# Kernel optimization log

Measured on AMD Instinct MI355X. Metric: run time of the kernel, lower is better.

Reference implementation:

```python
import jax, jax.numpy as jnp
import numpy as np

B, L, D, H = 2, 2048, 1024, 16
HD = D // H


def _xavier(key, out_f, in_f):
    std = (2.0 / (in_f + out_f)) ** 0.5
    return jax.random.normal(key, (out_f, in_f), dtype=jnp.float32) * std


def setup_inputs() -> dict:
    key = jax.random.key(0)
    k = jax.random.split(key, 8)
    Q = jax.random.normal(k[0], (B, L, D), dtype=jnp.float32)
    K = jax.random.normal(k[1], (B, L, D), dtype=jnp.float32)
    V = jax.random.normal(k[2], (B, L, D), dtype=jnp.float32)
    mask = jnp.tril(jnp.ones((L, L), dtype=jnp.int32))[None, None]  # causal [1,1,L,L]
    wq = _xavier(k[3], D, D)
    wk = _xavier(k[4], D, D)
    wv = _xavier(k[5], D, D)
    wo = _xavier(k[6], D, D)
    bo = jnp.zeros((D,), dtype=jnp.float32)
    return {"Q": Q, "K": K, "V": V, "mask": mask,
            "wq": wq, "wk": wk, "wv": wv, "wo": wo, "bo": bo}


def reference(Q, K, V, mask, wq, wk, wv, wo, bo):
    N, Lq, Dm = Q.shape
    # projections: X @ W^T (Linear stores [out, in])
    q = (Q @ wq.T).reshape(N, Lq, H, HD).transpose(0, 2, 1, 3)  # [N,H,L,hd]
    kk = (K @ wk.T).reshape(N, Lq, H, HD).transpose(0, 2, 1, 3)
    v = (V @ wv.T).reshape(N, Lq, H, HD).transpose(0, 2, 1, 3)
    score = jnp.einsum('bhqd,bhkd->bhqk', q, kk) / jnp.sqrt(jnp.float32(HD))
    score = jnp.where(mask == 0, -jnp.inf, score)
    weights = jax.nn.softmax(score, axis=-1)
    attn = jnp.einsum('bhqk,bhkd->bhqd', weights, v)
    out = attn.transpose(0, 2, 1, 3).reshape(N, Lq, Dm)
    return out @ wo.T + bo
```

## Files before the change

kernel.cpp:

```cpp
#include <hip/hip_runtime.h>
#include <hip/hip_bf16.h>


#define B_ 2
#define L_ 2048
#define D_ 1024
#define H_ 16
#define HD_ 64
#define NA_ ((size_t)B_ * L_ * D_)
#define NW_ ((size_t)D_ * D_)

typedef __attribute__((ext_vector_type(8))) short bf16x8;
typedef __attribute__((ext_vector_type(4))) float f32x4;
typedef __hip_bfloat16 bf16;

__device__ __forceinline__ void async_load16(const void* g, void* l) {
  __builtin_amdgcn_global_load_lds((const __attribute__((address_space(1))) void*)g,
                                   (__attribute__((address_space(3))) void*)l,
                                   16, 0, 0);
}

__global__ __launch_bounds__(256) void xcvt_kernel(const float* __restrict__ q,
                                                   const float* __restrict__ k,
                                                   const float* __restrict__ v,
                                                   const float* __restrict__ w0,
                                                   const float* __restrict__ w1,
                                                   const float* __restrict__ w2,
                                                   const float* __restrict__ w3,
                                                   bf16* __restrict__ dst) {
  const int y = blockIdx.y;
  const float* src = (y == 0) ? q : (y == 1) ? k : (y == 2) ? v
                   : (y == 3) ? w0 : (y == 4) ? w1 : (y == 5) ? w2 : w3;
  const size_t n = (y < 3) ? NA_ : NW_;
  const size_t off = (y < 3) ? (size_t)y * NA_ : 3 * NA_ + (size_t)(y - 3) * NW_;
  size_t i = ((size_t)blockIdx.x * 256 + threadIdx.x) * 4;
  if (i >= n) return;
  float4 vv = *(const float4*)(src + i);
  union { bf16 h[4]; uint2 u; } pk;
  pk.h[0] = __float2bfloat16(vv.x);
  pk.h[1] = __float2bfloat16(vv.y);
  pk.h[2] = __float2bfloat16(vv.z);
  pk.h[3] = __float2bfloat16(vv.w);
  *(uint2*)(dst + off + i) = pk.u;
}

__global__ __launch_bounds__(256) void gemm_qkv(const bf16* __restrict__ Qb,
                                                const bf16* __restrict__ Kb,
                                                const bf16* __restrict__ Vb,
                                                const bf16* __restrict__ Wb,
                                                bf16* __restrict__ qp,
                                                bf16* __restrict__ kp,
                                                bf16* __restrict__ vtp) {
  __shared__ __align__(16) bf16 As[128 * 32];
  __shared__ __align__(16) bf16 Bs[128 * 32];
  const int tid = threadIdx.x;
  const int wv = tid >> 6, lane = tid & 63;
  const int quad = lane >> 4, l16 = lane & 15;
  const int wm = wv & 1, wn = wv >> 1;
  const int m0 = blockIdx.x * 128, n0 = blockIdx.y * 128;
  const int z = blockIdx.z;
  const bf16* X = (z == 0) ? Qb : (z == 1) ? Kb : Vb;
  const bf16* W = Wb + (size_t)z * NW_;

  f32x4 acc[4][4];
#pragma unroll
  for (int i = 0; i < 4; i++)
#pragma unroll
    for (int j = 0; j < 4; j++) acc[i][j] = (f32x4){0.f, 0.f, 0.f, 0.f};

  for (int k0 = 0; k0 < D_; k0 += 32) {
#pragma unroll
    for (int it = 0; it < 2; it++) {
      int c = (wv * 2 + it) * 64 + lane;
      int row = c >> 2, cc = c & 3;
      async_load16(X + (size_t)(m0 + row) * D_ + k0 + cc * 8, (char*)As + c * 16);
      async_load16(W + (size_t)(n0 + row) * D_ + k0 + cc * 8, (char*)Bs + c * 16);
    }
    __syncthreads();
    bf16x8 af[4], bfr[4];
#pragma unroll
    for (int mi = 0; mi < 4; mi++)
      af[mi] = *(const bf16x8*)&As[(wm * 64 + mi * 16 + l16) * 32 + quad * 8];
#pragma unroll
    for (int ni = 0; ni < 4; ni++)
      bfr[ni] = *(const bf16x8*)&Bs[(wn * 64 + ni * 16 + l16) * 32 + quad * 8];
#pragma unroll
    for (int mi = 0; mi < 4; mi++)
#pragma unroll
      for (int ni = 0; ni < 4; ni++)
        acc[mi][ni] = __builtin_amdgcn_mfma_f32_16x16x32_bf16(af[mi], bfr[ni],
                                                              acc[mi][ni], 0, 0, 0);
    __syncthreads();
  }

  const float sc = (z == 0) ? 0.125f : 1.0f;
#pragma unroll
  for (int mi = 0; mi < 4; mi++) {
#pragma unroll
    for (int ni = 0; ni < 4; ni++) {
      int n = n0 + wn * 64 + ni * 16 + l16;
#pragma unroll
      for (int r = 0; r < 4; r++) {
        int m = m0 + wm * 64 + mi * 16 + quad * 4 + r;
        bf16 v = __float2bfloat16(acc[mi][ni][r] * sc);
        if (z == 2) {
          int b = m >> 11, l = m & (L_ - 1);
          int h = n >> 6, hd = n & 63;
          vtp[((size_t)((b * H_ + h) * HD_ + hd)) * L_ + l] = v;
        } else {
          ((z == 0) ? qp : kp)[(size_t)m * D_ + n] = v;
        }
      }
    }
  }
}

__global__ __launch_bounds__(256) void attn_kernel(const bf16* __restrict__ qp,
                                                   const bf16* __restrict__ kp,
                                                   const bf16* __restrict__ vt,
                                                   bf16* __restrict__ attn) {
  __shared__ __align__(16) bf16 Kt[2][64 * 64];
  __shared__ __align__(16) bf16 Vt[2][64 * 64];
  __shared__ __align__(16) bf16 Pl[4][16 * 72];
  __shared__ __align__(16) bf16 Ph[4][16 * 72];
  const int tid = threadIdx.x;
  const int wv = tid >> 6, lane = tid & 63;
  const int quad = lane >> 4, l16 = lane & 15;
  const int pair = blockIdx.x, h = blockIdx.y, b = blockIdx.z;
  const int qlo = pair, qhi = (L_ / 64 - 1) - pair;

  const int rL = qlo * 64 + wv * 16 + l16;
  const int rH = qhi * 64 + wv * 16 + l16;
  bf16x8 qaL[2], qaH[2];
#pragma unroll
  for (int kk = 0; kk < 2; kk++) {
    qaL[kk] = *(const bf16x8*)&qp[((size_t)(b * L_ + rL)) * D_ + h * HD_ +
                                  kk * 32 + quad * 8];
    qaH[kk] = *(const bf16x8*)&qp[((size_t)(b * L_ + rH)) * D_ + h * HD_ +
                                  kk * 32 + quad * 8];
  }

  f32x4 OL[4], OH[4];
#pragma unroll
  for (int t = 0; t < 4; t++) {
    OL[t] = (f32x4){0.f, 0.f, 0.f, 0.f};
    OH[t] = (f32x4){0.f, 0.f, 0.f, 0.f};
  }
  float lL[4] = {0.f, 0.f, 0.f, 0.f}, lH[4] = {0.f, 0.f, 0.f, 0.f};

  const int csw = quad ^ (l16 & 7);

  auto stage = [&](int j, int buf) {
    const int j0 = j * 64;
#pragma unroll
    for (int it = 0; it < 2; it++) {
      int slot = (wv * 2 + it) * 64 + lane;
      int row = slot >> 3, c = (slot & 7) ^ (row & 7);
      async_load16(kp + ((size_t)(b * L_ + j0 + row)) * D_ + h * HD_ + c * 8,
                   (char*)Kt[buf] + slot * 16);
      async_load16(vt + ((size_t)((b * H_ + h) * HD_ + row)) * L_ + j0 + c * 8,
                   (char*)Vt[buf] + slot * 16);
    }
  };

  stage(0, 0);
  for (int j = 0; j <= qhi; j++) {
    const int buf = j & 1;
    const int j0 = j * 64;
    const bool doLo = (j <= qlo);
    __syncthreads();
    if (j < qhi) stage(j + 1, buf ^ 1);

    f32x4 sL[4], sH[4];
#pragma unroll
    for (int ss = 0; ss < 4; ss++) {
      int krow = ss * 16 + l16;
      bf16x8 kb0 = *(const bf16x8*)&Kt[buf][krow * 64 + csw * 8];
      bf16x8 kb1 = *(const bf16x8*)&Kt[buf][krow * 64 + (csw ^ 4) * 8];
      f32x4 s = (f32x4){0.f, 0.f, 0.f, 0.f};
      s = __builtin_amdgcn_mfma_f32_16x16x32_bf16(qaH[0], kb0, s, 0, 0, 0);
      s = __builtin_amdgcn_mfma_f32_16x16x32_bf16(qaH[1], kb1, s, 0, 0, 0);
      sH[ss] = s;
      if (doLo) {
        f32x4 t = (f32x4){0.f, 0.f, 0.f, 0.f};
        t = __builtin_amdgcn_mfma_f32_16x16x32_bf16(qaL[0], kb0, t, 0, 0, 0);
        t = __builtin_amdgcn_mfma_f32_16x16x32_bf16(qaL[1], kb1, t, 0, 0, 0);
        sL[ss] = t;
      }
    }

    if (j == qhi) {
#pragma unroll
      for (int ss = 0; ss < 4; ss++) {
        int key = j0 + ss * 16 + l16;
#pragma unroll
        for (int r = 0; r < 4; r++) {
          int rq = qhi * 64 + wv * 16 + quad * 4 + r;
          if (key > rq) sH[ss][r] = -1e30f;
        }
      }
    }
    if (doLo && j == qlo) {
#pragma unroll
      for (int ss = 0; ss < 4; ss++) {
        int key = j0 + ss * 16 + l16;
#pragma unroll
        for (int r = 0; r < 4; r++) {
          int rq = qlo * 64 + wv * 16 + quad * 4 + r;
          if (key > rq) sL[ss][r] = -1e30f;
        }
      }
    }
#pragma unroll
    for (int ss = 0; ss < 4; ss++) {
#pragma unroll
      for (int r = 0; r < 4; r++) {
        float p = __expf(sH[ss][r]);
        lH[r] += p;
        Ph[wv][(quad * 4 + r) * 72 + ss * 16 + l16] = __float2bfloat16(p);
      }
    }
    if (doLo) {
#pragma unroll
      for (int ss = 0; ss < 4; ss++) {
#pragma unroll
        for (int r = 0; r < 4; r++) {
          float p = __expf(sL[ss][r]);
          lL[r] += p;
          Pl[wv][(quad * 4 + r) * 72 + ss * 16 + l16] = __float2bfloat16(p);
        }
      }
    }

    asm volatile("s_waitcnt lgkmcnt(0)" ::: "memory");

#pragma unroll
    for (int kk = 0; kk < 2; kk++) {
      bf16x8 pah = *(const bf16x8*)&Ph[wv][l16 * 72 + kk * 32 + quad * 8];
      bf16x8 pal;
      if (doLo) pal = *(const bf16x8*)&Pl[wv][l16 * 72 + kk * 32 + quad * 8];
#pragma unroll
      for (int t = 0; t < 4; t++) {
        bf16x8 vb = *(const bf16x8*)&Vt[buf][(t * 16 + l16) * 64 + (csw ^ (kk * 4)) * 8];
        OH[t] = __builtin_amdgcn_mfma_f32_16x16x32_bf16(pah, vb, OH[t], 0, 0, 0);
        if (doLo) OL[t] = __builtin_amdgcn_mfma_f32_16x16x32_bf16(pal, vb, OL[t], 0, 0, 0);
      }
    }
  }

#pragma unroll
  for (int r = 0; r < 4; r++) {
#pragma unroll
    for (int off = 1; off < 16; off <<= 1) {
      lL[r] += __shfl_xor(lL[r], off, 64);
      lH[r] += __shfl_xor(lH[r], off, 64);
    }
  }
#pragma unroll
  for (int t = 0; t < 4; t++) {
#pragma unroll
    for (int r = 0; r < 4; r++) {
      int rowL = qlo * 64 + wv * 16 + quad * 4 + r;
      int rowH = qhi * 64 + wv * 16 + quad * 4 + r;
      attn[((size_t)(b * L_ + rowL)) * D_ + h * HD_ + t * 16 + l16] =
          __float2bfloat16(OL[t][r] / lL[r]);
      attn[((size_t)(b * L_ + rowH)) * D_ + h * HD_ + t * 16 + l16] =
          __float2bfloat16(OH[t][r] / lH[r]);
    }
  }
}

__global__ __launch_bounds__(256) void gemm_out(const bf16* __restrict__ X,
                                                const bf16* __restrict__ W,
                                                const float* __restrict__ bias,
                                                float* __restrict__ out) {
  __shared__ __align__(16) bf16 As[64 * 32];
  __shared__ __align__(16) bf16 Bs[128 * 32];
  const int tid = threadIdx.x;
  const int wv = tid >> 6, lane = tid & 63;
  const int quad = lane >> 4, l16 = lane & 15;
  const int wm = wv & 1, wn = wv >> 1;
  const int m0 = blockIdx.x * 64, n0 = blockIdx.y * 128;

  f32x4 acc[2][4];
#pragma unroll
  for (int i = 0; i < 2; i++)
#pragma unroll
    for (int j = 0; j < 4; j++) acc[i][j] = (f32x4){0.f, 0.f, 0.f, 0.f};

  for (int k0 = 0; k0 < D_; k0 += 32) {
    {
      int c = tid;
      int row = c >> 2, cc = c & 3;
      async_load16(X + (size_t)(m0 + row) * D_ + k0 + cc * 8, (char*)As + c * 16);
    }
#pragma unroll
    for (int it = 0; it < 2; it++) {
      int c = (wv * 2 + it) * 64 + lane;
      int row = c >> 2, cc = c & 3;
      async_load16(W + (size_t)(n0 + row) * D_ + k0 + cc * 8, (char*)Bs + c * 16);
    }
    __syncthreads();
    bf16x8 af[2], bfr[4];
#pragma unroll
    for (int mi = 0; mi < 2; mi++)
      af[mi] = *(const bf16x8*)&As[(wm * 32 + mi * 16 + l16) * 32 + quad * 8];
#pragma unroll
    for (int ni = 0; ni < 4; ni++)
      bfr[ni] = *(const bf16x8*)&Bs[(wn * 64 + ni * 16 + l16) * 32 + quad * 8];
#pragma unroll
    for (int mi = 0; mi < 2; mi++)
#pragma unroll
      for (int ni = 0; ni < 4; ni++)
        acc[mi][ni] = __builtin_amdgcn_mfma_f32_16x16x32_bf16(af[mi], bfr[ni],
                                                              acc[mi][ni], 0, 0, 0);
    __syncthreads();
  }

#pragma unroll
  for (int mi = 0; mi < 2; mi++) {
#pragma unroll
    for (int ni = 0; ni < 4; ni++) {
      int n = n0 + wn * 64 + ni * 16 + l16;
      float bval = bias[n];
#pragma unroll
      for (int r = 0; r < 4; r++) {
        int m = m0 + wm * 32 + mi * 16 + quad * 4 + r;
        out[(size_t)m * D_ + n] = acc[mi][ni][r] + bval;
      }
    }
  }
}

extern "C" void kernel_launch(void* const* d_in, const int* in_sizes, int n_in,
                              void* d_out, int out_size, void* d_ws, size_t ws_size,
                              hipStream_t stream) {
  const float* Q  = (const float*)d_in[0];
  const float* K  = (const float*)d_in[1];
  const float* V  = (const float*)d_in[2];
  const float* wq = (const float*)d_in[4];
  const float* wk = (const float*)d_in[5];
  const float* wvp = (const float*)d_in[6];
  const float* wo = (const float*)d_in[7];
  const float* bo = (const float*)d_in[8];
  float* out = (float*)d_out;

  bf16* base = (bf16*)d_ws;
  bf16* Qb = base;
  bf16* Kb = Qb + NA_;
  bf16* Vb = Kb + NA_;
  bf16* Wb = Vb + NA_;
  bf16* qp = Wb + 4 * NW_;
  bf16* kp = qp + NA_;
  bf16* vt = kp + NA_;
  bf16* at = vt + NA_;

  xcvt_kernel<<<dim3(NA_ / 1024, 7), 256, 0, stream>>>(Q, K, V, wq, wk, wvp, wo, base);
  gemm_qkv<<<dim3(32, 8, 3), 256, 0, stream>>>(Qb, Kb, Vb, Wb, qp, kp, vt);
  attn_kernel<<<dim3(L_ / 128, H_, B_), 256, 0, stream>>>(qp, kp, vt, at);
  gemm_out<<<dim3(64, 8), 256, 0, stream>>>(at, Wb + 3 * NW_, bo, out);
}
```

Measured before the change: 239.5 us.

## Load K/V tiles directly into registers in attention, drop LDS staging and barriers

```diff
diff --git a/kernel.cpp b/kernel.cpp
--- a/kernel.cpp
+++ b/kernel.cpp
@@ -115,12 +115,10 @@
   }
 }
 
-__global__ __launch_bounds__(256) void attn_kernel(const bf16* __restrict__ qp,
-                                                   const bf16* __restrict__ kp,
-                                                   const bf16* __restrict__ vt,
-                                                   bf16* __restrict__ attn) {
-  __shared__ __align__(16) bf16 Kt[2][64 * 64];
-  __shared__ __align__(16) bf16 Vt[2][64 * 64];
+__global__ __launch_bounds__(256, 2) void attn_kernel(const bf16* __restrict__ qp,
+                                                      const bf16* __restrict__ kp,
+                                                      const bf16* __restrict__ vt,
+                                                      bf16* __restrict__ attn) {
   __shared__ __align__(16) bf16 Pl[4][16 * 72];
   __shared__ __align__(16) bf16 Ph[4][16 * 72];
   const int tid = threadIdx.x;
@@ -129,15 +127,15 @@
   const int pair = blockIdx.x, h = blockIdx.y, b = blockIdx.z;
   const int qlo = pair, qhi = (L_ / 64 - 1) - pair;
 
-  const int rL = qlo * 64 + wv * 16 + l16;
-  const int rH = qhi * 64 + wv * 16 + l16;
+  const int rLq = qlo * 64 + wv * 16 + l16;
+  const int rHq = qhi * 64 + wv * 16 + l16;
   bf16x8 qaL[2], qaH[2];
 #pragma unroll
-  for (int kk = 0; kk < 2; kk++) {
-    qaL[kk] = *(const bf16x8*)&qp[((size_t)(b * L_ + rL)) * D_ + h * HD_ +
-                                  kk * 32 + quad * 8];
-    qaH[kk] = *(const bf16x8*)&qp[((size_t)(b * L_ + rH)) * D_ + h * HD_ +
-                                  kk * 32 + quad * 8];
+  for (int c = 0; c < 2; c++) {
+    qaL[c] = *(const bf16x8*)&qp[((size_t)(b * L_ + rLq)) * D_ + h * HD_ +
+                                 c * 32 + quad * 8];
+    qaH[c] = *(const bf16x8*)&qp[((size_t)(b * L_ + rHq)) * D_ + h * HD_ +
+                                 c * 32 + quad * 8];
   }
 
   f32x4 OL[4], OH[4];
@@ -146,94 +144,107 @@
     OL[t] = (f32x4){0.f, 0.f, 0.f, 0.f};
     OH[t] = (f32x4){0.f, 0.f, 0.f, 0.f};
   }
-  float lL[4] = {0.f, 0.f, 0.f, 0.f}, lH[4] = {0.f, 0.f, 0.f, 0.f};
-
-  const int csw = quad ^ (l16 & 7);
-
-  auto stage = [&](int j, int buf) {
-    const int j0 = j * 64;
-#pragma unroll
-    for (int it = 0; it < 2; it++) {
-      int slot = (wv * 2 + it) * 64 + lane;
-      int row = slot >> 3, c = (slot & 7) ^ (row & 7);
-      async_load16(kp + ((size_t)(b * L_ + j0 + row)) * D_ + h * HD_ + c * 8,
-                   (char*)Kt[buf] + slot * 16);
-      async_load16(vt + ((size_t)((b * H_ + h) * HD_ + row)) * L_ + j0 + c * 8,
-                   (char*)Vt[buf] + slot * 16);
-    }
-  };
-
-  stage(0, 0);
+  float lL = 0.f, lH = 0.f;
+
+  const bf16* kbase = kp + ((size_t)b * L_) * D_ + h * HD_;
+  const bf16* vbase = vt + ((size_t)(b * H_ + h) * HD_) * L_;
+
+  bf16x8 kc[8];
+#pragma unroll
+  for (int ss = 0; ss < 4; ss++)
+#pragma unroll
+    for (int c = 0; c < 2; c++)
+      kc[ss * 2 + c] = *(const bf16x8*)&kbase[((size_t)(ss * 16 + l16)) * D_ +
+                                              c * 32 + quad * 8];
+
   for (int j = 0; j <= qhi; j++) {
-    const int buf = j & 1;
     const int j0 = j * 64;
     const bool doLo = (j <= qlo);
-    __syncthreads();
-    if (j < qhi) stage(j + 1, buf ^ 1);
-
-    f32x4 sL[4], sH[4];
+
+    bf16x8 vb[8];
+#pragma unroll
+    for (int t = 0; t < 4; t++)
+#pragma unroll
+      for (int kk = 0; kk < 2; kk++)
+        vb[t * 2 + kk] = *(const bf16x8*)&vbase[((size_t)(t * 16 + l16)) * L_ +
+                                                j0 + kk * 32 + quad * 8];
+
+    f32x4 sH[4], sL[4];
+    __builtin_amdgcn_s_setprio(1);
 #pragma unroll
     for (int ss = 0; ss < 4; ss++) {
-      int krow = ss * 16 + l16;
-      bf16x8 kb0 = *(const bf16x8*)&Kt[buf][krow * 64 + csw * 8];
-      bf16x8 kb1 = *(const bf16x8*)&Kt[buf][krow * 64 + (csw ^ 4) * 8];
       f32x4 s = (f32x4){0.f, 0.f, 0.f, 0.f};
-      s = __builtin_amdgcn_mfma_f32_16x16x32_bf16(qaH[0], kb0, s, 0, 0, 0);
-      s = __builtin_amdgcn_mfma_f32_16x16x32_bf16(qaH[1], kb1, s, 0, 0, 0);
+      s = __builtin_amdgcn_mfma_f32_16x16x32_bf16(kc[ss * 2 + 0], qaH[0], s, 0, 0, 0);
+      s = __builtin_amdgcn_mfma_f32_16x16x32_bf16(kc[ss * 2 + 1], qaH[1], s, 0, 0, 0);
       sH[ss] = s;
       if (doLo) {
-        f32x4 t = (f32x4){0.f, 0.f, 0.f, 0.f};
-        t = __builtin_amdgcn_mfma_f32_16x16x32_bf16(qaL[0], kb0, t, 0, 0, 0);
-        t = __builtin_amdgcn_mfma_f32_16x16x32_bf16(qaL[1], kb1, t, 0, 0, 0);
-        sL[ss] = t;
-      }
+        f32x4 t2 = (f32x4){0.f, 0.f, 0.f, 0.f};
+        t2 = __builtin_amdgcn_mfma_f32_16x16x32_bf16(kc[ss * 2 + 0], qaL[0], t2, 0, 0, 0);
+        t2 = __builtin_amdgcn_mfma_f32_16x16x32_bf16(kc[ss * 2 + 1], qaL[1], t2, 0, 0, 0);
+        sL[ss] = t2;
+      }
+    }
+    __builtin_amdgcn_s_setprio(0);
+
+    if (j < qhi) {
+      const int j1 = j0 + 64;
+#pragma unroll
+      for (int ss = 0; ss < 4; ss++)
+#pragma unroll
+        for (int c = 0; c < 2; c++)
+          kc[ss * 2 + c] = *(const bf16x8*)&kbase[((size_t)(j1 + ss * 16 + l16)) * D_ +
+                                                  c * 32 + quad * 8];
     }
 
     if (j == qhi) {
 #pragma unroll
+      for (int ss = 0; ss < 4; ss++)
+#pragma unroll
+        for (int r = 0; r < 4; r++) {
+          int key = j0 + ss * 16 + quad * 4 + r;
+          if (key > rHq) sH[ss][r] = -1e30f;
+        }
+    }
+    if (doLo && j == qlo) {
+#pragma unroll
+      for (int ss = 0; ss < 4; ss++)
+#pragma unroll
+        for (int r = 0; r < 4; r++) {
+          int key = j0 + ss * 16 + quad * 4 + r;
+          if (key > rLq) sL[ss][r] = -1e30f;
+        }
+    }
+
+#pragma unroll
+    for (int ss = 0; ss < 4; ss++) {
+      float p0 = __expf(sH[ss][0]), p1 = __expf(sH[ss][1]);
+      float p2 = __expf(sH[ss][2]), p3 = __expf(sH[ss][3]);
+      lH += (p0 + p1) + (p2 + p3);
+      union { bf16 hx[4]; uint2 d; } pk;
+      pk.hx[0] = __float2bfloat16(p0);
+      pk.hx[1] = __float2bfloat16(p1);
+      pk.hx[2] = __float2bfloat16(p2);
+      pk.hx[3] = __float2bfloat16(p3);
+      *(uint2*)&Ph[wv][l16 * 72 + ss * 16 + quad * 4] = pk.d;
+    }
+    if (doLo) {
+#pragma unroll
       for (int ss = 0; ss < 4; ss++) {
-        int key = j0 + ss * 16 + l16;
-#pragma unroll
-        for (int r = 0; r < 4; r++) {
-          int rq = qhi * 64 + wv * 16 + quad * 4 + r;
-          if (key > rq) sH[ss][r] = -1e30f;
-        }
-      }
-    }
-    if (doLo && j == qlo) {
-#pragma unroll
-      for (int ss = 0; ss < 4; ss++) {
-        int key = j0 + ss * 16 + l16;
-#pragma unroll
-        for (int r = 0; r < 4; r++) {
-          int rq = qlo * 64 + wv * 16 + quad * 4 + r;
-          if (key > rq) sL[ss][r] = -1e30f;
-        }
-      }
-    }
-#pragma unroll
-    for (int ss = 0; ss < 4; ss++) {
-#pragma unroll
-      for (int r = 0; r < 4; r++) {
-        float p = __expf(sH[ss][r]);
-        lH[r] += p;
-        Ph[wv][(quad * 4 + r) * 72 + ss * 16 + l16] = __float2bfloat16(p);
-      }
-    }
-    if (doLo) {
-#pragma unroll
-      for (int ss = 0; ss < 4; ss++) {
-#pragma unroll
-        for (int r = 0; r < 4; r++) {
-          float p = __expf(sL[ss][r]);
-          lL[r] += p;
-          Pl[wv][(quad * 4 + r) * 72 + ss * 16 + l16] = __float2bfloat16(p);
-        }
+        float p0 = __expf(sL[ss][0]), p1 = __expf(sL[ss][1]);
+        float p2 = __expf(sL[ss][2]), p3 = __expf(sL[ss][3]);
+        lL += (p0 + p1) + (p2 + p3);
+        union { bf16 hx[4]; uint2 d; } pk;
+        pk.hx[0] = __float2bfloat16(p0);
+        pk.hx[1] = __float2bfloat16(p1);
+        pk.hx[2] = __float2bfloat16(p2);
+        pk.hx[3] = __float2bfloat16(p3);
+        *(uint2*)&Pl[wv][l16 * 72 + ss * 16 + quad * 4] = pk.d;
       }
     }
 
     asm volatile("s_waitcnt lgkmcnt(0)" ::: "memory");
 
+    __builtin_amdgcn_s_setprio(1);
 #pragma unroll
     for (int kk = 0; kk < 2; kk++) {
       bf16x8 pah = *(const bf16x8*)&Ph[wv][l16 * 72 + kk * 32 + quad * 8];
@@ -241,20 +252,22 @@
       if (doLo) pal = *(const bf16x8*)&Pl[wv][l16 * 72 + kk * 32 + quad * 8];
 #pragma unroll
       for (int t = 0; t < 4; t++) {
-        bf16x8 vb = *(const bf16x8*)&Vt[buf][(t * 16 + l16) * 64 + (csw ^ (kk * 4)) * 8];
-        OH[t] = __builtin_amdgcn_mfma_f32_16x16x32_bf16(pah, vb, OH[t], 0, 0, 0);
-        if (doLo) OL[t] = __builtin_amdgcn_mfma_f32_16x16x32_bf16(pal, vb, OL[t], 0, 0, 0);
-      }
-    }
-  }
-
+        OH[t] = __builtin_amdgcn_mfma_f32_16x16x32_bf16(pah, vb[t * 2 + kk], OH[t], 0, 0, 0);
+        if (doLo) OL[t] = __builtin_amdgcn_mfma_f32_16x16x32_bf16(pal, vb[t * 2 + kk], OL[t], 0, 0, 0);
+      }
+    }
+    __builtin_amdgcn_s_setprio(0);
+  }
+
+  lL += __shfl_xor(lL, 16, 64);
+  lL += __shfl_xor(lL, 32, 64);
+  lH += __shfl_xor(lH, 16, 64);
+  lH += __shfl_xor(lH, 32, 64);
+  float lLq[4], lHq[4];
 #pragma unroll
   for (int r = 0; r < 4; r++) {
-#pragma unroll
-    for (int off = 1; off < 16; off <<= 1) {
-      lL[r] += __shfl_xor(lL[r], off, 64);
-      lH[r] += __shfl_xor(lH[r], off, 64);
-    }
+    lLq[r] = __shfl(lL, quad * 4 + r, 64);
+    lHq[r] = __shfl(lH, quad * 4 + r, 64);
   }
 #pragma unroll
   for (int t = 0; t < 4; t++) {
@@ -263,9 +276,9 @@
       int rowL = qlo * 64 + wv * 16 + quad * 4 + r;
       int rowH = qhi * 64 + wv * 16 + quad * 4 + r;
       attn[((size_t)(b * L_ + rowL)) * D_ + h * HD_ + t * 16 + l16] =
-          __float2bfloat16(OL[t][r] / lL[r]);
+          __float2bfloat16(OL[t][r] / lLq[r]);
       attn[((size_t)(b * L_ + rowH)) * D_ + h * HD_ + t * 16 + l16] =
-          __float2bfloat16(OH[t][r] / lH[r]);
+          __float2bfloat16(OH[t][r] / lHq[r]);
     }
   }
 }
```

After: 298.9 us. 1.25x slower.
